# Performance work log

Measured on AMD Instinct MI355X. Metric: run time of the kernel, lower is better.

## Reference

```python
import jax, jax.numpy as jnp
import numpy as np
from jax import lax

DN = ('NCHW', 'OIHW', 'NCHW')
BN_EPS = 1e-5
LRELU_SLOPE = 0.01


def conv_block(x, w1, b1, w2, b2, gamma, bn_bias):
    # Conv2d(512->256, k=1) -> Conv2d(256->512, k=3, pad=1) -> LeakyReLU -> BatchNorm2d(512)
    y = lax.conv_general_dilated(x, w1, (1, 1), 'VALID', dimension_numbers=DN)
    y = y + b1[None, :, None, None]
    y = lax.conv_general_dilated(y, w2, (1, 1), 'SAME', dimension_numbers=DN)
    y = y + b2[None, :, None, None]
    y = jnp.where(y > 0, y, LRELU_SLOPE * y)
    # BatchNorm2d in training mode: batch statistics over (B, H, W) per channel
    mean = jnp.mean(y, axis=(0, 2, 3))
    var = jnp.var(y, axis=(0, 2, 3))
    y = (y - mean[None, :, None, None]) * lax.rsqrt(var + BN_EPS)[None, :, None, None]
    return y * gamma[None, :, None, None] + bn_bias[None, :, None, None]


def setup_inputs() -> dict:
    key = jax.random.key(0)
    ks = jax.random.split(key, 9)
    B, C, H, W = 8, 512, 32, 32
    x = jax.random.normal(ks[0], (B, C, H, W), dtype=jnp.float32)
    x1 = jax.random.normal(ks[1], (B, C, H, W), dtype=jnp.float32)
    x2 = jax.random.normal(ks[2], (B, C, H, W), dtype=jnp.float32)
    w1 = jax.random.normal(ks[3], (256, 512, 1, 1), dtype=jnp.float32) * 0.02
    b1 = jnp.zeros((256,), dtype=jnp.float32)
    w2 = jax.random.normal(ks[4], (512, 256, 3, 3), dtype=jnp.float32) * 0.02
    b2 = jnp.zeros((512,), dtype=jnp.float32)
    gamma = jnp.ones((512,), dtype=jnp.float32)
    bn_bias = jnp.zeros((512,), dtype=jnp.float32)
    beta = jax.random.normal(ks[5], (1,), dtype=jnp.float32)  # Parameter(zeros(1)) in torch; random so output is non-trivial
    return {"x": x, "x1": x1, "x2": x2, "w1": w1, "b1": b1, "w2": w2,
            "b2": b2, "gamma": gamma, "bn_bias": bn_bias, "beta": beta}


def reference(x, x1, x2, w1, b1, w2, b2, gamma, bn_bias, beta):
    B, C, H, W = x1.shape
    N = H * W
    F1 = conv_block(x1, w1, b1, w2, b2, gamma, bn_bias).reshape(B, C, N)   # [B, C, N]
    F2 = conv_block(x2, w1, b1, w2, b2, gamma, bn_bias).reshape(B, C, N)   # [B, C, N]
    scores = jnp.einsum('bcn,bdn->bcd', F1, F2)                            # [B, C, C]
    attention = jax.nn.softmax(scores, axis=-1)
    out = jnp.einsum('bcd,bdn->bcn', attention, x.reshape(B, C, N))
    return beta * out.reshape(B, C, H, W)
```

## Files before the change

### kernel.cpp

```cpp
#include <hip/hip_runtime.h>


typedef __attribute__((ext_vector_type(8))) short bfrag;
typedef __attribute__((ext_vector_type(4))) float facc;
typedef __attribute__((ext_vector_type(16))) float facc16;

__device__ __forceinline__ unsigned short bf16_rn(float v) {
  unsigned u = __float_as_uint(v);
  return (unsigned short)((u + 0x7fffu + ((u >> 16) & 1u)) >> 16);
}

__global__ __launch_bounds__(256) void prep_w2(const float* __restrict__ w2,
                                               unsigned short* __restrict__ hi,
                                               unsigned short* __restrict__ lo,
                                               float* __restrict__ statsz) {
  if (blockIdx.x < 40) statsz[blockIdx.x * 256 + threadIdx.x] = 0.f;
  int co = blockIdx.x;
  int ci = threadIdx.x;
  const float* src = w2 + ((size_t)co * 256 + ci) * 9;
#pragma unroll
  for (int tap = 0; tap < 9; tap++) {
    float v = src[tap];
    unsigned short h = bf16_rn(v);
    float fh = __uint_as_float((unsigned)h << 16);
    unsigned short l = bf16_rn(v - fh);
    size_t idx = ((size_t)tap * 512 + co) * 256 + ci;
    hi[idx] = h;
    lo[idx] = l;
  }
}

__global__ __launch_bounds__(256) void transpose_split(
    const float* __restrict__ src0, const float* __restrict__ src1,
    unsigned short* __restrict__ hi, unsigned short* __restrict__ lo) {
  __shared__ float tile[32][33];
  int z = blockIdx.z;
  const float* src = (z < 8) ? src0 + (size_t)z * 524288 : src1 + (size_t)(z - 8) * 524288;
  int ci0 = blockIdx.y * 32, p0 = blockIdx.x * 32;
  int t = threadIdx.x;
  {
    int ci_l = t >> 5, p_l = t & 31;
#pragma unroll
    for (int j = 0; j < 4; j++)
      tile[ci_l + 8 * j][p_l] = src[(size_t)(ci0 + ci_l + 8 * j) * 1024 + p0 + p_l];
  }
  __syncthreads();
  {
    int p_l = t >> 3, cg = (t & 7) * 4;
    unsigned short hh[4], ll[4];
#pragma unroll
    for (int j = 0; j < 4; j++) {
      float v = tile[cg + j][p_l];
      hh[j] = bf16_rn(v);
      ll[j] = bf16_rn(v - __uint_as_float((unsigned)hh[j] << 16));
    }
    size_t idx = ((size_t)z * 1024 + p0 + p_l) * 512 + ci0 + cg;
    *(ushort4*)(hi + idx) = make_ushort4(hh[0], hh[1], hh[2], hh[3]);
    *(ushort4*)(lo + idx) = make_ushort4(ll[0], ll[1], ll[2], ll[3]);
  }
}

template <int KTOT, int EPI, int AF32, int KSPLIT>
__global__ __launch_bounds__(256, 2) void gemm_nt(
    const void* __restrict__ Ahi_, const unsigned short* __restrict__ Alo,
    int aLD, long long aBS,
    const unsigned short* __restrict__ Bhi, const unsigned short* __restrict__ Blo,
    int bLD, long long bBS,
    void* __restrict__ out0, void* __restrict__ out1,
    const float* __restrict__ p0, const float* __restrict__ p1,
    const float* __restrict__ p2, const float* __restrict__ p3) {
  __shared__ __attribute__((aligned(16))) unsigned char smem[65536];
  int t = threadIdx.x;
  int z = blockIdx.z;
  int zb = z, kh = 0;
  if (KSPLIT) { zb = z & 7; kh = z >> 3; }
  int m0 = blockIdx.y * 128, n0 = blockIdx.x * 128;
  int w = t >> 6, lane = t & 63;
  int lm = lane & 15, q = lane >> 4;
  int mh = (w & 1) * 64, nh = (w >> 1) * 64;
  facc acc[4][4] = {};
  for (int k0 = 0; k0 < KTOT; k0 += 64) {
    __syncthreads();
    if (AF32) {
      const float* Af = (const float*)Ahi_ + (size_t)zb * aBS;
#pragma unroll
      for (int j = 0; j < 8; j++) {
        int idx = t + 256 * j;
        int row = idx >> 4, c4 = idx & 15;
        float4 v = *(const float4*)(Af + (size_t)(m0 + row) * aLD + k0 + c4 * 4);
        unsigned short h0 = bf16_rn(v.x), h1 = bf16_rn(v.y), h2 = bf16_rn(v.z), h3 = bf16_rn(v.w);
        unsigned short l0 = bf16_rn(v.x - __uint_as_float((unsigned)h0 << 16));
        unsigned short l1 = bf16_rn(v.y - __uint_as_float((unsigned)h1 << 16));
        unsigned short l2 = bf16_rn(v.z - __uint_as_float((unsigned)h2 << 16));
        unsigned short l3 = bf16_rn(v.w - __uint_as_float((unsigned)h3 << 16));
        int base = row * 256 + (((c4 >> 1) ^ (row & 7)) * 16) + (c4 & 1) * 8;
        *(ushort4*)(smem + base) = make_ushort4(h0, h1, h2, h3);
        *(ushort4*)(smem + base + 128) = make_ushort4(l0, l1, l2, l3);
      }
    } else {
      const unsigned short* Ah = (const unsigned short*)Ahi_ + (size_t)zb * aBS + kh * KTOT;
      const unsigned short* Al = Alo + (size_t)zb * aBS + kh * KTOT;
#pragma unroll
      for (int j = 0; j < 8; j++) {
        int idx = t + 256 * j;
        int row = idx >> 4, c = idx & 15;
        const unsigned short* src = (c < 8) ? Ah : Al;
        uint4 v = *(const uint4*)(src + (size_t)(m0 + row) * aLD + k0 + (c & 7) * 8);
        *(uint4*)(smem + row * 256 + ((((c & 7) ^ (row & 7)) | (c & 8)) * 16)) = v;
      }
    }
#pragma unroll
    for (int j = 0; j < 8; j++) {
      int idx = t + 256 * j;
      int row = idx >> 4, c = idx & 15;
      const unsigned short* src = (c < 8) ? Bhi : Blo;
      uint4 v = *(const uint4*)(src + (size_t)zb * bBS + (size_t)kh * KTOT +
                                (size_t)(n0 + row) * bLD + k0 + (c & 7) * 8);
      *(uint4*)(smem + 32768 + row * 256 + ((((c & 7) ^ (row & 7)) | (c & 8)) * 16)) = v;
    }
    __syncthreads();
#pragma unroll
    for (int ks = 0; ks < 2; ks++) {
      bfrag ah[4], al[4], bh[4], bl[4];
#pragma unroll
      for (int mt = 0; mt < 4; mt++) {
        int m = mh + mt * 16 + lm;
        int phys = ((ks * 4 + q) ^ (m & 7)) * 16;
        const unsigned char* p = smem + m * 256;
        ah[mt] = *(const bfrag*)(p + phys);
        al[mt] = *(const bfrag*)(p + phys + 128);
      }
#pragma unroll
      for (int nt = 0; nt < 4; nt++) {
        int n = nh + nt * 16 + lm;
        int phys = ((ks * 4 + q) ^ (n & 7)) * 16;
        const unsigned char* p = smem + 32768 + n * 256;
        bh[nt] = *(const bfrag*)(p + phys);
        bl[nt] = *(const bfrag*)(p + phys + 128);
      }
#pragma unroll
      for (int mt = 0; mt < 4; mt++)
#pragma unroll
        for (int nt = 0; nt < 4; nt++) {
          acc[mt][nt] = __builtin_amdgcn_mfma_f32_16x16x32_bf16(ah[mt], bh[nt], acc[mt][nt], 0, 0, 0);
          acc[mt][nt] = __builtin_amdgcn_mfma_f32_16x16x32_bf16(ah[mt], bl[nt], acc[mt][nt], 0, 0, 0);
          acc[mt][nt] = __builtin_amdgcn_mfma_f32_16x16x32_bf16(al[mt], bh[nt], acc[mt][nt], 0, 0, 0);
        }
    }
  }
  if (EPI == 0) {
    unsigned short* Oh = (unsigned short*)out0;
    unsigned short* Ol = (unsigned short*)out1;
#pragma unroll
    for (int mt = 0; mt < 4; mt++) {
      int mb = m0 + mh + mt * 16 + q * 4;
#pragma unroll
      for (int nt = 0; nt < 4; nt++) {
        int n = n0 + nh + nt * 16 + lm;
        unsigned short hh[4], ll[4];
#pragma unroll
        for (int r = 0; r < 4; r++) {
          float v = acc[mt][nt][r] + p0[mb + r];
          hh[r] = bf16_rn(v);
          ll[r] = bf16_rn(v - __uint_as_float((unsigned)hh[r] << 16));
        }
        size_t o = ((size_t)(zb * 1024 + n)) * 256 + mb;
        *(ushort4*)(Oh + o) = make_ushort4(hh[0], hh[1], hh[2], hh[3]);
        *(ushort4*)(Ol + o) = make_ushort4(ll[0], ll[1], ll[2], ll[3]);
      }
    }
  } else if (EPI == 1) {
    float* S = (float*)out0 + (size_t)kh * 2097152;
    const float* stats = p0;
    const float* rowsum = p1;
    const float* gamma = p2;
    const float* bnb = p3;
    float a2v[4], t2v[4], r2v[4];
#pragma unroll
    for (int nt = 0; nt < 4; nt++) {
      int d = n0 + nh + nt * 16 + lm;
      float mu = stats[512 + d] * (1.f / 8192.f);
      float var = stats[1536 + d] * (1.f / 8192.f) - mu * mu;
      float a = gamma[d] * rsqrtf(var + 1e-5f);
      a2v[nt] = a;
      t2v[nt] = bnb[d] - mu * a;
      r2v[nt] = rowsum[(8 + zb) * 512 + d];
    }
#pragma unroll
    for (int mt = 0; mt < 4; mt++)
#pragma unroll
      for (int r = 0; r < 4; r++) {
        int c = m0 + mh + mt * 16 + q * 4 + r;
        float mu = stats[c] * (1.f / 8192.f);
        float var = stats[1024 + c] * (1.f / 8192.f) - mu * mu;
        float a1 = gamma[c] * rsqrtf(var + 1e-5f);
        float t1 = bnb[c] - mu * a1;
        float r1 = rowsum[zb * 512 + c];
#pragma unroll
        for (int nt = 0; nt < 4; nt++) {
          int d = n0 + nh + nt * 16 + lm;
          float sc = a1 * a2v[nt] * acc[mt][nt][r];
          if (kh == 0)
            sc += a1 * t2v[nt] * r1 + t1 * a2v[nt] * r2v[nt] + 1024.f * t1 * t2v[nt];
          S[((size_t)(zb * 512 + c)) * 512 + d] = sc;
        }
      }
  } else {
    float* O = (float*)out0;
    float sc = p0[0];
#pragma unroll
    for (int mt = 0; mt < 4; mt++)
#pragma unroll
      for (int r = 0; r < 4; r++) {
        int c = m0 + mh + mt * 16 + q * 4 + r;
#pragma unroll
        for (int nt = 0; nt < 4; nt++) {
          int n = n0 + nh + nt * 16 + lm;
          O[((size_t)(zb * 512 + c)) * 1024 + n] = sc * acc[mt][nt][r];
        }
      }
  }
}

__global__ __launch_bounds__(512, 2) void conv3x3_mfma512(
    const unsigned short* __restrict__ Y1thi, const unsigned short* __restrict__ Y1tlo,
    const unsigned short* __restrict__ w2bhi, const unsigned short* __restrict__ w2blo,
    const float* __restrict__ b2, unsigned short* __restrict__ Fhi,
    unsigned short* __restrict__ Flo, float* __restrict__ stats,
    float* __restrict__ rowsum) {
  __shared__ __attribute__((aligned(16))) unsigned char smem[95488];
  const int WOFF = 21760;
  int t = threadIdx.x;
  int g = blockIdx.z;
  int co_base = blockIdx.y * 128;
  int y0 = blockIdx.x * 8;
  int w = t >> 6, l = t & 63;
  int l31 = l & 31, q2 = l >> 5;
  int co_half = (w & 1) * 64;
  int row_base = (w >> 1) * 2;
  facc16 acc[2][2] = {};
  for (int c16 = 0; c16 < 16; c16++) {
    int ci0 = c16 * 16;
    __syncthreads();
    for (int u = t; u < 1360; u += 512) {
      int e = u >> 2, c = u & 3;
      int srow = e / 34, sx = e - srow * 34;
      int gy = y0 - 1 + srow, gx = sx - 1;
      uint4 v = make_uint4(0u, 0u, 0u, 0u);
      if ((unsigned)gy < 32u && (unsigned)gx < 32u) {
        const unsigned short* src = (c < 2) ? Y1thi : Y1tlo;
        v = *(const uint4*)(src + (size_t)((g * 32 + gy) * 32 + gx) * 256 + ci0 + (c & 1) * 8);
      }
      *(uint4*)(smem + e * 64 + ((c ^ ((e >> 1) & 3)) << 4)) = v;
    }
    for (int u = t; u < 4608; u += 512) {
      int e = u >> 2, c = u & 3;
      int tap = e >> 7, co = e & 127;
      const unsigned short* src = (c < 2) ? w2bhi : w2blo;
      uint4 v = *(const uint4*)(src + (size_t)(tap * 512 + co_base + co) * 256 + ci0 + (c & 1) * 8);
      *(uint4*)(smem + WOFF + e * 64 + ((c ^ ((e >> 1) & 3)) << 4)) = v;
    }
    __syncthreads();
#pragma unroll
    for (int tap = 0; tap < 9; tap++) {
      const int dy = tap / 3, dx = tap % 3;
      bfrag ah[2], al[2], bh[2], bl[2];
#pragma unroll
      for (int jt = 0; jt < 2; jt++) {
        int cr = co_half + jt * 32 + l31;
        int ew = tap * 128 + cr;
        int off = WOFF + ew * 64 + ((q2 ^ ((ew >> 1) & 3)) << 4);
        ah[jt] = *(const bfrag*)(smem + off);
        al[jt] = *(const bfrag*)(smem + (off ^ 32));
      }
#pragma unroll
      for (int it = 0; it < 2; it++) {
        int ei = (row_base + it + dy) * 34 + l31 + dx;
        int off = ei * 64 + ((q2 ^ ((ei >> 1) & 3)) << 4);
        bh[it] = *(const bfrag*)(smem + off);
        bl[it] = *(const bfrag*)(smem + (off ^ 32));
      }
#pragma unroll
      for (int jt = 0; jt < 2; jt++)
#pragma unroll
        for (int it = 0; it < 2; it++) {
          acc[jt][it] = __builtin_amdgcn_mfma_f32_32x32x16_bf16(ah[jt], bh[it], acc[jt][it], 0, 0, 0);
          acc[jt][it] = __builtin_amdgcn_mfma_f32_32x32x16_bf16(ah[jt], bl[it], acc[jt][it], 0, 0, 0);
          acc[jt][it] = __builtin_amdgcn_mfma_f32_32x32x16_bf16(al[jt], bh[it], acc[jt][it], 0, 0, 0);
        }
    }
  }
  int grp = g >> 3;
  int pxg0 = blockIdx.x * 256 + (w >> 1) * 64;
#pragma unroll
  for (int jt = 0; jt < 2; jt++)
#pragma unroll
    for (int r = 0; r < 16; r++) {
      int co = co_base + co_half + jt * 32 + (r & 3) + 8 * (r >> 2) + 4 * q2;
      float bb = b2[co];
      float s = 0.f, s2 = 0.f;
#pragma unroll
      for (int it = 0; it < 2; it++) {
        float v = acc[jt][it][r] + bb;
        v = v > 0.f ? v : 0.01f * v;
        unsigned short h = bf16_rn(v);
        unsigned short lo_ = bf16_rn(v - __uint_as_float((unsigned)h << 16));
        size_t o = (size_t)(g * 512 + co) * 1024 + pxg0 + it * 32 + l31;
        Fhi[o] = h;
        Flo[o] = lo_;
        s += v;
        s2 = fmaf(v, v, s2);
      }
#pragma unroll
      for (int d = 1; d <= 16; d <<= 1) {
        s += __shfl_xor(s, d);
        s2 += __shfl_xor(s2, d);
      }
      if (l31 == 0) {
        atomicAdd(&stats[grp * 512 + co], s);
        atomicAdd(&stats[1024 + grp * 512 + co], s2);
        atomicAdd(&rowsum[g * 512 + co], s);
      }
    }
}

__global__ __launch_bounds__(256) void softmax_rows(float* __restrict__ S) {
  int row = blockIdx.x;
  float* p = S + (size_t)row * 512;
  const float* p1 = p + 2097152;
  int t = threadIdx.x;
  float2 va = *(const float2*)(p + 2 * t);
  float2 vb = *(const float2*)(p1 + 2 * t);
  float vx = va.x + vb.x, vy = va.y + vb.y;
  float mx = fmaxf(vx, vy);
#pragma unroll
  for (int d = 32; d >= 1; d >>= 1) mx = fmaxf(mx, __shfl_xor(mx, d));
  __shared__ float sred[8];
  int wave = t >> 6, lane = t & 63;
  if (lane == 0) sred[wave] = mx;
  __syncthreads();
  float m4 = fmaxf(fmaxf(sred[0], sred[1]), fmaxf(sred[2], sred[3]));
  float ex = expf(vx - m4), ey = expf(vy - m4);
  float s = ex + ey;
#pragma unroll
  for (int d = 32; d >= 1; d >>= 1) s += __shfl_xor(s, d);
  if (lane == 0) sred[4 + wave] = s;
  __syncthreads();
  float inv = 1.f / (sred[4] + sred[5] + sred[6] + sred[7]);
  float px_ = ex * inv, py_ = ey * inv;
  unsigned short h0 = bf16_rn(px_), h1 = bf16_rn(py_);
  unsigned short l0 = bf16_rn(px_ - __uint_as_float((unsigned)h0 << 16));
  unsigned short l1 = bf16_rn(py_ - __uint_as_float((unsigned)h1 << 16));
  unsigned short* rh = (unsigned short*)p;
  *(ushort2*)(rh + 2 * t) = make_ushort2(h0, h1);
  *(ushort2*)(rh + 512 + 2 * t) = make_ushort2(l0, l1);
}

extern "C" void kernel_launch(void* const* d_in, const int* in_sizes, int n_in,
                              void* d_out, int out_size, void* d_ws, size_t ws_size,
                              hipStream_t stream) {
  const float* x = (const float*)d_in[0];
  const float* x1 = (const float*)d_in[1];
  const float* x2 = (const float*)d_in[2];
  const float* w1 = (const float*)d_in[3];
  const float* b1 = (const float*)d_in[4];
  const float* w2 = (const float*)d_in[5];
  const float* b2 = (const float*)d_in[6];
  const float* gamma = (const float*)d_in[7];
  const float* bnb = (const float*)d_in[8];
  const float* beta = (const float*)d_in[9];
  float* out = (float*)d_out;
  float* ws = (float*)d_ws;

  unsigned short* x12thi = (unsigned short*)ws;
  unsigned short* x12tlo = (unsigned short*)(ws + 4194304);
  unsigned short* Fhi = (unsigned short*)ws;
  unsigned short* Flo = (unsigned short*)(ws + 4194304);
  unsigned short* xthi = (unsigned short*)ws;
  unsigned short* xtlo = (unsigned short*)(ws + 2097152);
  unsigned short* Y1thi = (unsigned short*)(ws + 8388608);
  unsigned short* Y1tlo = (unsigned short*)(ws + 10485760);
  float* S = ws + 8388608;
  unsigned short* w2bhi = (unsigned short*)(ws + 12582912);
  unsigned short* w2blo = (unsigned short*)(ws + 13172736);
  float* stats = ws + 13762560;
  float* rowsum = ws + 13764608;

  prep_w2<<<512, 256, 0, stream>>>(w2, w2bhi, w2blo, stats);
  transpose_split<<<dim3(32, 16, 16), 256, 0, stream>>>(x1, x2, x12thi, x12tlo);
  gemm_nt<512, 0, 1, 0><<<dim3(8, 2, 16), 256, 0, stream>>>(
      w1, nullptr, 512, 0LL, x12thi, x12tlo, 512, 524288LL,
      Y1thi, Y1tlo, b1, nullptr, nullptr, nullptr);
  conv3x3_mfma512<<<dim3(4, 4, 16), 512, 0, stream>>>(
      Y1thi, Y1tlo, w2bhi, w2blo, b2, Fhi, Flo, stats, rowsum);
  gemm_nt<512, 1, 0, 1><<<dim3(4, 4, 16), 256, 0, stream>>>(
      Fhi, Flo, 1024, 524288LL, Fhi + (size_t)8 * 524288, Flo + (size_t)8 * 524288,
      1024, 524288LL, S, nullptr, stats, rowsum, gamma, bnb);
  transpose_split<<<dim3(32, 16, 8), 256, 0, stream>>>(x, x, xthi, xtlo);
  softmax_rows<<<4096, 256, 0, stream>>>(S);
  gemm_nt<512, 2, 0, 0><<<dim3(8, 4, 8), 256, 0, stream>>>(
      (unsigned short*)S, (unsigned short*)S + 512, 1024, 524288LL,
      xthi, xtlo, 512, 524288LL, out, nullptr, beta, nullptr, nullptr, nullptr);
}
```

Baseline: 354.6 us.

## Software-pipeline 3x3 conv with register-prefetched weights and smaller 4-row tiles

Rewrites the 3x3 conv kernel to stage weights one kernel row (dy) at a time and inputs in 32-channel chunks. The next stage's global loads are prefetched into registers while MFMAs consume the current shared-memory tile, so load latency overlaps compute. Blocks shrink to 256 threads covering 4 output rows, which doubles the grid and cuts shared memory so more blocks fit per CU. The cost is more barriers, more register pressure from the prefetch buffers, and a larger input halo relative to the tile, so more input rows are reloaded.

```diff
diff --git a/kernel.cpp b/kernel.cpp
--- a/kernel.cpp
+++ b/kernel.cpp
@@ -190,19 +190,19 @@
     for (int mt = 0; mt < 4; mt++)
 #pragma unroll
       for (int r = 0; r < 4; r++) {
-        int c = m0 + mh + mt * 16 + q * 4 + r;
-        float mu = stats[c] * (1.f / 8192.f);
-        float var = stats[1024 + c] * (1.f / 8192.f) - mu * mu;
-        float a1 = gamma[c] * rsqrtf(var + 1e-5f);
-        float t1 = bnb[c] - mu * a1;
-        float r1 = rowsum[zb * 512 + c];
+        int cc = m0 + mh + mt * 16 + q * 4 + r;
+        float mu = stats[cc] * (1.f / 8192.f);
+        float var = stats[1024 + cc] * (1.f / 8192.f) - mu * mu;
+        float a1 = gamma[cc] * rsqrtf(var + 1e-5f);
+        float t1 = bnb[cc] - mu * a1;
+        float r1 = rowsum[zb * 512 + cc];
 #pragma unroll
         for (int nt = 0; nt < 4; nt++) {
           int d = n0 + nh + nt * 16 + lm;
           float sc = a1 * a2v[nt] * acc[mt][nt][r];
           if (kh == 0)
             sc += a1 * t2v[nt] * r1 + t1 * a2v[nt] * r2v[nt] + 1024.f * t1 * t2v[nt];
-          S[((size_t)(zb * 512 + c)) * 512 + d] = sc;
+          S[((size_t)(zb * 512 + cc)) * 512 + d] = sc;
         }
       }
   } else {
@@ -212,100 +212,147 @@
     for (int mt = 0; mt < 4; mt++)
 #pragma unroll
       for (int r = 0; r < 4; r++) {
-        int c = m0 + mh + mt * 16 + q * 4 + r;
+        int cc = m0 + mh + mt * 16 + q * 4 + r;
 #pragma unroll
         for (int nt = 0; nt < 4; nt++) {
           int n = n0 + nh + nt * 16 + lm;
-          O[((size_t)(zb * 512 + c)) * 1024 + n] = sc * acc[mt][nt][r];
-        }
-      }
-  }
-}
-
-__global__ __launch_bounds__(512, 2) void conv3x3_mfma512(
+          O[((size_t)(zb * 512 + cc)) * 1024 + n] = sc * acc[mt][nt][r];
+        }
+      }
+  }
+}
+
+__global__ __launch_bounds__(256, 2) void conv3x3_pipe(
     const unsigned short* __restrict__ Y1thi, const unsigned short* __restrict__ Y1tlo,
     const unsigned short* __restrict__ w2bhi, const unsigned short* __restrict__ w2blo,
     const float* __restrict__ b2, unsigned short* __restrict__ Fhi,
     unsigned short* __restrict__ Flo, float* __restrict__ stats,
     float* __restrict__ rowsum) {
-  __shared__ __attribute__((aligned(16))) unsigned char smem[95488];
-  const int WOFF = 21760;
+  __shared__ __attribute__((aligned(16))) unsigned char smem[75264];
+  const int WOFF = 26112;
+  const int WSTRIDE = 393216;
   int t = threadIdx.x;
-  int g = blockIdx.z;
-  int co_base = blockIdx.y * 128;
-  int y0 = blockIdx.x * 8;
-  int w = t >> 6, l = t & 63;
-  int l31 = l & 31, q2 = l >> 5;
+  int g = blockIdx.z, co_base = blockIdx.y * 128, y0 = blockIdx.x * 4;
+  int w = t >> 6, lane = t & 63;
+  int l31 = lane & 31, q2 = lane >> 5;
   int co_half = (w & 1) * 64;
-  int row_base = (w >> 1) * 2;
+  int rb = (w >> 1) * 2;
+
+  int c = t & 7;
+  int e0 = t >> 3;
+  const unsigned short* wbase =
+      ((c < 4) ? w2bhi : w2blo) + ((size_t)(co_base + e0) * 256 + (c & 3) * 8);
+  int wlds0 = WOFF + e0 * 128 + ((c ^ (e0 & 7)) << 4);
+  const unsigned short* isel = ((c < 4) ? Y1thi : Y1tlo) + (c & 3) * 8;
+  int ioff[7], ilds[7];
+  bool ivalid[7], iexists[7];
+#pragma unroll
+  for (int j = 0; j < 7; j++) {
+    int e = e0 + 32 * j;
+    int srow = e / 34, sx = e - srow * 34;
+    int gy = y0 - 1 + srow, gx = sx - 1;
+    iexists[j] = e < 204;
+    ivalid[j] = iexists[j] && ((unsigned)gy < 32u) && ((unsigned)gx < 32u);
+    ioff[j] = ivalid[j] ? ((g * 32 + gy) * 32 + gx) * 256 : 0;
+    ilds[j] = e * 128 + ((c ^ (e & 7)) << 4);
+  }
+  int selA0 = (q2 ^ (l31 & 7)) << 4;
+  int selA1 = ((2 + q2) ^ (l31 & 7)) << 4;
+
+#pragma unroll
+  for (int j = 0; j < 12; j++)
+    *(uint4*)(smem + wlds0 + j * 4096) =
+        *(const uint4*)(wbase + (j >> 2) * 131072 + (j & 3) * 8192);
+#pragma unroll
+  for (int j = 0; j < 7; j++) {
+    if (iexists[j]) {
+      uint4 v = make_uint4(0u, 0u, 0u, 0u);
+      if (ivalid[j]) v = *(const uint4*)(isel + ioff[j]);
+      *(uint4*)(smem + ilds[j]) = v;
+    }
+  }
+  __syncthreads();
+
   facc16 acc[2][2] = {};
-  for (int c16 = 0; c16 < 16; c16++) {
-    int ci0 = c16 * 16;
-    __syncthreads();
-    for (int u = t; u < 1360; u += 512) {
-      int e = u >> 2, c = u & 3;
-      int srow = e / 34, sx = e - srow * 34;
-      int gy = y0 - 1 + srow, gx = sx - 1;
-      uint4 v = make_uint4(0u, 0u, 0u, 0u);
-      if ((unsigned)gy < 32u && (unsigned)gx < 32u) {
-        const unsigned short* src = (c < 2) ? Y1thi : Y1tlo;
-        v = *(const uint4*)(src + (size_t)((g * 32 + gy) * 32 + gx) * 256 + ci0 + (c & 1) * 8);
-      }
-      *(uint4*)(smem + e * 64 + ((c ^ ((e >> 1) & 3)) << 4)) = v;
-    }
-    for (int u = t; u < 4608; u += 512) {
-      int e = u >> 2, c = u & 3;
-      int tap = e >> 7, co = e & 127;
-      const unsigned short* src = (c < 2) ? w2bhi : w2blo;
-      uint4 v = *(const uint4*)(src + (size_t)(tap * 512 + co_base + co) * 256 + ci0 + (c & 1) * 8);
-      *(uint4*)(smem + WOFF + e * 64 + ((c ^ ((e >> 1) & 3)) << 4)) = v;
-    }
-    __syncthreads();
-#pragma unroll
-    for (int tap = 0; tap < 9; tap++) {
-      const int dy = tap / 3, dx = tap % 3;
-      bfrag ah[2], al[2], bh[2], bl[2];
-#pragma unroll
-      for (int jt = 0; jt < 2; jt++) {
-        int cr = co_half + jt * 32 + l31;
-        int ew = tap * 128 + cr;
-        int off = WOFF + ew * 64 + ((q2 ^ ((ew >> 1) & 3)) << 4);
-        ah[jt] = *(const bfrag*)(smem + off);
-        al[jt] = *(const bfrag*)(smem + (off ^ 32));
-      }
-#pragma unroll
-      for (int it = 0; it < 2; it++) {
-        int ei = (row_base + it + dy) * 34 + l31 + dx;
-        int off = ei * 64 + ((q2 ^ ((ei >> 1) & 3)) << 4);
-        bh[it] = *(const bfrag*)(smem + off);
-        bl[it] = *(const bfrag*)(smem + (off ^ 32));
-      }
-#pragma unroll
-      for (int jt = 0; jt < 2; jt++)
-#pragma unroll
-        for (int it = 0; it < 2; it++) {
-          acc[jt][it] = __builtin_amdgcn_mfma_f32_32x32x16_bf16(ah[jt], bh[it], acc[jt][it], 0, 0, 0);
-          acc[jt][it] = __builtin_amdgcn_mfma_f32_32x32x16_bf16(ah[jt], bl[it], acc[jt][it], 0, 0, 0);
-          acc[jt][it] = __builtin_amdgcn_mfma_f32_32x32x16_bf16(al[jt], bh[it], acc[jt][it], 0, 0, 0);
-        }
+  uint4 wreg[12], inreg[7];
+  for (int chunk = 0; chunk < 8; chunk++) {
+    int ci0 = chunk * 32;
+#pragma unroll
+    for (int dy = 0; dy < 3; dy++) {
+      bool last = (dy == 2) && (chunk == 7);
+      if (!last) {
+        int ndy = (dy == 2) ? 0 : dy + 1;
+        int nci = (dy == 2) ? ci0 + 32 : ci0;
+        const unsigned short* wp = wbase + ndy * WSTRIDE + nci;
+#pragma unroll
+        for (int j = 0; j < 12; j++)
+          wreg[j] = *(const uint4*)(wp + (j >> 2) * 131072 + (j & 3) * 8192);
+        if (dy == 2) {
+#pragma unroll
+          for (int j = 0; j < 7; j++) {
+            inreg[j] = make_uint4(0u, 0u, 0u, 0u);
+            if (ivalid[j]) inreg[j] = *(const uint4*)(isel + ioff[j] + nci);
+          }
+        }
+      }
+#pragma unroll
+      for (int dx = 0; dx < 3; dx++) {
+#pragma unroll
+        for (int s = 0; s < 2; s++) {
+          int selA = s ? selA1 : selA0;
+          int kc = s * 2 + q2;
+          bfrag ah[2], al[2], bh[2], bl[2];
+#pragma unroll
+          for (int ct = 0; ct < 2; ct++) {
+            int off = WOFF + (dx * 128 + co_half + ct * 32 + l31) * 128 + selA;
+            ah[ct] = *(const bfrag*)(smem + off);
+            al[ct] = *(const bfrag*)(smem + (off ^ 64));
+          }
+#pragma unroll
+          for (int it = 0; it < 2; it++) {
+            int ei = (rb + it + dy) * 34 + l31 + dx;
+            int off = ei * 128 + ((kc ^ (ei & 7)) << 4);
+            bh[it] = *(const bfrag*)(smem + off);
+            bl[it] = *(const bfrag*)(smem + (off ^ 64));
+          }
+#pragma unroll
+          for (int ct = 0; ct < 2; ct++)
+#pragma unroll
+            for (int it = 0; it < 2; it++) {
+              acc[ct][it] = __builtin_amdgcn_mfma_f32_32x32x16_bf16(ah[ct], bh[it], acc[ct][it], 0, 0, 0);
+              acc[ct][it] = __builtin_amdgcn_mfma_f32_32x32x16_bf16(ah[ct], bl[it], acc[ct][it], 0, 0, 0);
+              acc[ct][it] = __builtin_amdgcn_mfma_f32_32x32x16_bf16(al[ct], bh[it], acc[ct][it], 0, 0, 0);
+            }
+        }
+      }
+      __syncthreads();
+      if (!last) {
+#pragma unroll
+        for (int j = 0; j < 12; j++) *(uint4*)(smem + wlds0 + j * 4096) = wreg[j];
+        if (dy == 2) {
+#pragma unroll
+          for (int j = 0; j < 7; j++)
+            if (iexists[j]) *(uint4*)(smem + ilds[j]) = inreg[j];
+        }
+        __syncthreads();
+      }
     }
   }
   int grp = g >> 3;
-  int pxg0 = blockIdx.x * 256 + (w >> 1) * 64;
-#pragma unroll
-  for (int jt = 0; jt < 2; jt++)
+#pragma unroll
+  for (int ct = 0; ct < 2; ct++)
 #pragma unroll
     for (int r = 0; r < 16; r++) {
-      int co = co_base + co_half + jt * 32 + (r & 3) + 8 * (r >> 2) + 4 * q2;
+      int co = co_base + co_half + ct * 32 + (r & 3) + 8 * (r >> 2) + 4 * q2;
       float bb = b2[co];
       float s = 0.f, s2 = 0.f;
 #pragma unroll
       for (int it = 0; it < 2; it++) {
-        float v = acc[jt][it][r] + bb;
+        float v = acc[ct][it][r] + bb;
         v = v > 0.f ? v : 0.01f * v;
         unsigned short h = bf16_rn(v);
         unsigned short lo_ = bf16_rn(v - __uint_as_float((unsigned)h << 16));
-        size_t o = (size_t)(g * 512 + co) * 1024 + pxg0 + it * 32 + l31;
+        size_t o = (size_t)(g * 512 + co) * 1024 + (y0 + rb + it) * 32 + l31;
         Fhi[o] = h;
         Flo[o] = lo_;
         s += v;
@@ -391,7 +438,7 @@
   gemm_nt<512, 0, 1, 0><<<dim3(8, 2, 16), 256, 0, stream>>>(
       w1, nullptr, 512, 0LL, x12thi, x12tlo, 512, 524288LL,
       Y1thi, Y1tlo, b1, nullptr, nullptr, nullptr);
-  conv3x3_mfma512<<<dim3(4, 4, 16), 512, 0, stream>>>(
+  conv3x3_pipe<<<dim3(8, 4, 16), 256, 0, stream>>>(
       Y1thi, Y1tlo, w2bhi, w2blo, b2, Fhi, Flo, stats, rowsum);
   gemm_nt<512, 1, 0, 1><<<dim3(4, 4, 16), 256, 0, stream>>>(
       Fhi, Flo, 1024, 524288LL, Fhi + (size_t)8 * 524288, Flo + (size_t)8 * 524288,
```

Measured after the change: 480.1 us. +35.4%, slower.
